# Kernel tuning notes

Hardware: AMD Instinct MI355X
Metric: run time of the kernel (lower is better)

Reference implementation:

```python
import jax, jax.numpy as jnp
import numpy as np
import math

EMBED_DIM = 1024
N1 = 8192
N2 = 8192

def setup_inputs() -> dict:
    key = jax.random.key(0)
    ks = jax.random.split(key, 16)
    D = EMBED_DIM
    s = 1.0 / math.sqrt(D)
    inp = {
        "input_tensor1": jax.random.normal(ks[0], (N1, D), jnp.float32),
        "input_tensor2": jax.random.normal(ks[1], (N2, D), jnp.float32),
    }
    names = ["q1", "k1", "v1", "q2", "k2", "v2"]
    for i, n in enumerate(names):
        inp[f"W{n}"] = jax.random.normal(ks[2 + 2 * i], (D, D), jnp.float32) * s
        inp[f"b{n}"] = jax.random.normal(ks[3 + 2 * i], (D,), jnp.float32) * 0.01
    return inp

def reference(input_tensor1, input_tensor2,
              Wq1, bq1, Wk1, bk1, Wv1, bv1,
              Wq2, bq2, Wk2, bk2, Wv2, bv2):
    D = Wq1.shape[0]
    scale = 1.0 / math.sqrt(D)
    # projections (torch Linear: x @ W^T + b; here W stored pre-transposed)
    q1 = input_tensor1 @ Wq1 + bq1   # [N1, D]
    k1 = input_tensor1 @ Wk1 + bk1   # [N1, D]
    v1 = input_tensor1 @ Wv1 + bv1   # [N1, D]
    q2 = input_tensor2 @ Wq2 + bq2   # [N2, D]
    k2 = input_tensor2 @ Wk2 + bk2   # [N2, D]
    v2 = input_tensor2 @ Wv2 + bv2   # [N2, D]
    # direction 1: tensor2 queries attend to tensor1 keys/values
    probs1 = jax.nn.sigmoid((q2 @ k1.T) * scale)   # [N2, N1]
    ctx1 = probs1 @ v1                              # [N2, D]
    # direction 2: tensor1 queries attend to tensor2 keys/values
    probs2 = jax.nn.sigmoid((q1 @ k2.T) * scale)   # [N1, N2]
    ctx2 = probs2 @ v2                              # [N1, D]
    return (ctx2, probs2, ctx1, probs1)
```

## Files before the change

### kernel.cpp

```cpp
#include <hip/hip_runtime.h>
#include <hip/hip_bf16.h>

#define DIM   1024
#define NTOK  8192

using bf16 = __hip_bfloat16;
typedef __attribute__((ext_vector_type(8))) short bf16x8;
typedef __attribute__((ext_vector_type(4))) float f32x4;

__device__ __forceinline__ unsigned short f2b(float x) {
  union { __hip_bfloat16 h; unsigned short u; } cv;
  cv.h = __float2bfloat16(x);
  return cv.u;
}

__global__ __launch_bounds__(256) void cast_f32_bf16(const float* __restrict__ in,
                                                     bf16* __restrict__ out, int n4) {
  int i = blockIdx.x * 256 + threadIdx.x;
  if (i < n4) {
    const float4 v = ((const float4*)in)[i];
    ushort4 p;
    p.x = f2b(v.x); p.y = f2b(v.y); p.z = f2b(v.z); p.w = f2b(v.w);
    ((ushort4*)out)[i] = p;
  }
}

__global__ __launch_bounds__(256) void transpose_cast32(const float* __restrict__ in,
                                                        bf16* __restrict__ out, int R, int C) {
  __shared__ float t[32][33];
  const int tilesC = C / 32;
  const int c0 = (blockIdx.x % tilesC) * 32;
  const int r0 = (blockIdx.x / tilesC) * 32;
  const int tx = threadIdx.x & 31, ty = threadIdx.x >> 5;
  #pragma unroll
  for (int i = 0; i < 4; ++i) {
    int r = ty + i * 8;
    t[r][tx] = in[(size_t)(r0 + r) * C + c0 + tx];
  }
  __syncthreads();
  #pragma unroll
  for (int i = 0; i < 4; ++i) {
    int cr = ty + i * 8;
    out[(size_t)(c0 + cr) * R + r0 + tx] = __float2bfloat16(t[tx][cr]);
  }
}

__global__ __launch_bounds__(256) void transpose_bf16(const short* __restrict__ in,
                                                      short* __restrict__ out,
                                                      const short* __restrict__ in2,
                                                      short* __restrict__ out2,
                                                      int R, int C) {
  __shared__ short t[64][72];
  const int tilesC = C >> 6;
  const int tilesPer = (R >> 6) * tilesC;
  int bid = blockIdx.x;
  const short* src = in; short* dst = out;
  if (bid >= tilesPer) { bid -= tilesPer; src = in2; dst = out2; }
  const int r0 = (bid / tilesC) << 6, c0 = (bid % tilesC) << 6;
  const int tr = threadIdx.x >> 3, tc8 = (threadIdx.x & 7) << 3;
  #pragma unroll
  for (int p = 0; p < 2; ++p) {
    int r = tr + p * 32;
    int sc = tc8 ^ (((r >> 3) & 7) << 3);
    *(bf16x8*)&t[r][sc] = *(const bf16x8*)&src[(size_t)(r0 + r) * C + c0 + tc8];
  }
  __syncthreads();
  #pragma unroll
  for (int p = 0; p < 2; ++p) {
    int oc = tr + p * 32;
    bf16x8 v;
    #pragma unroll
    for (int e = 0; e < 8; ++e) {
      int a = tc8 + e;
      v[e] = t[a][oc ^ (((a >> 3) & 7) << 3)];
    }
    *(bf16x8*)&dst[(size_t)(c0 + oc) * R + r0 + tc8] = v;
  }
}

__global__ __launch_bounds__(256) void pack_bias(const float* b0, const float* b1,
                                                 const float* b2, const float* b3,
                                                 const float* b4, const float* b5,
                                                 float* __restrict__ out) {
  int i = blockIdx.x * 256 + threadIdx.x;
  if (i < 6 * DIM) {
    int s = i >> 10, o = i & 1023;
    const float* p = (s == 0) ? b0 : (s == 1) ? b1 : (s == 2) ? b2 : (s == 3) ? b3 : (s == 4) ? b4 : b5;
    out[i] = p[o];
  }
}

template<int EPI, bool DUAL>
__global__ __launch_bounds__(256, 3) void gemm128(
    const bf16* __restrict__ A,  const bf16* __restrict__ Bt,
    const bf16* __restrict__ A2, const bf16* __restrict__ Bt2,
    int M, int N, int K, int TM, int perDir,
    const float* __restrict__ bias, const float* __restrict__ bias2, float scale,
    float* __restrict__ Cf, float* __restrict__ Cf2,
    bf16* __restrict__ Cb, bf16* __restrict__ Cb2,
    bf16* __restrict__ Cq, bf16* __restrict__ Ck, bf16* __restrict__ Cv,
    bf16* __restrict__ Cq2, bf16* __restrict__ Ck2, bf16* __restrict__ Cv2)
{
  __shared__ __align__(16) char smem[49152];
  bf16* sA = (bf16*)smem;
  bf16* sB = (bf16*)(smem + 24576);
  float* Lf = (float*)smem;

  const int t    = threadIdx.x;
  const int lane = t & 63, wid = t >> 6;
  const int wr = wid >> 1, wc = wid & 1;
  const int lr = lane & 15, kg = lane >> 4;

  const int nwg = gridDim.x;
  int bid = blockIdx.x;
  { const int q = nwg >> 3; bid = (bid & 7) * q + (bid >> 3); }

  const bf16* Au = A; const bf16* BtU = Bt;
  float* CfU = Cf; bf16* CbU = Cb;
  if (DUAL && bid >= perDir) { bid -= perDir; Au = A2; BtU = Bt2; CfU = Cf2; CbU = Cb2; }

  const int gw = TM << 3;
  const int s  = bid / gw, w = bid % gw;
  const int bm = (w >> 3) << 7;
  const int bn = ((s << 3) + (w & 7)) << 7;

  const float* biasU = bias;
  bf16 *CqU = Cq, *CkU = Ck, *CvU = Cv;
  int bmL = bm;
  if (EPI == 5 && bm >= (M >> 1)) {
    BtU = Bt2; biasU = bias2; CqU = Cq2; CkU = Ck2; CvU = Cv2; bmL = bm - (M >> 1);
  }

  const int srow = t >> 2;
  const int scol = ((t & 3) ^ ((t >> 3) & 3)) * 8;
  const size_t gA = (size_t)(bm + srow) * K + scol;
  const size_t gB = (size_t)(bn + srow) * K + scol;

#define STAGE(slot, isB, R0, tt_) \
  __builtin_amdgcn_global_load_lds( \
    (const __attribute__((address_space(1))) unsigned int*)(((isB) ? BtU + gB : Au + gA) + (size_t)(R0) * K + (size_t)(tt_) * 32), \
    (__attribute__((address_space(3))) unsigned int*)(((isB) ? sB : sA) + (slot) * 4096 + (R0) * 32 + t * 8), \
    16, 0, 0)

  const int swz  = (kg ^ ((lr >> 1) & 3)) * 8;
  const int aoff = (wr * 64 + lr) * 32 + swz;
  const int boff = (wc * 64 + lr) * 32 + swz;

  f32x4 acc[4][4] = {};
  const int NT = K >> 5;

  STAGE(0, 0, 0, 0); STAGE(0, 0, 64, 0); STAGE(0, 1, 0, 0); STAGE(0, 1, 64, 0);
  STAGE(1, 0, 0, 1); STAGE(1, 0, 64, 1); STAGE(1, 1, 0, 1); STAGE(1, 1, 64, 1);
  asm volatile("s_waitcnt vmcnt(4)" ::: "memory");
  __builtin_amdgcn_sched_barrier(0);
  __builtin_amdgcn_s_barrier();

  int cur = 0, stg = 2;
  for (int tt = 0; tt < NT; ++tt) {
    bf16x8 a[4], b[4];
    const bf16* pa = sA + cur * 4096 + aoff;
    const bf16* pb = sB + cur * 4096 + boff;
    #pragma unroll
    for (int i = 0; i < 4; ++i) a[i] = *(const bf16x8*)(pa + i * 512);
    #pragma unroll
    for (int i = 0; i < 4; ++i) b[i] = *(const bf16x8*)(pb + i * 512);
    if (tt + 2 < NT) {
      STAGE(stg, 0, 0, tt + 2); STAGE(stg, 0, 64, tt + 2);
      STAGE(stg, 1, 0, tt + 2); STAGE(stg, 1, 64, tt + 2);
    }
    __builtin_amdgcn_s_barrier();
    asm volatile("s_waitcnt lgkmcnt(0)" ::: "memory");
    __builtin_amdgcn_sched_barrier(0);
    __builtin_amdgcn_s_setprio(1);
    #pragma unroll
    for (int mi = 0; mi < 4; ++mi)
      #pragma unroll
      for (int n = 0; n < 4; ++n)
        acc[mi][n] = __builtin_amdgcn_mfma_f32_16x16x32_bf16(a[mi], b[n], acc[mi][n], 0, 0, 0);
    __builtin_amdgcn_s_setprio(0);
    if (tt + 2 < NT) { asm volatile("s_waitcnt vmcnt(4)" ::: "memory"); }
    else             { asm volatile("s_waitcnt vmcnt(0)" ::: "memory"); }
    __builtin_amdgcn_sched_barrier(0);
    __builtin_amdgcn_s_barrier();
    cur = (cur == 2) ? 0 : cur + 1;
    stg = (stg == 2) ? 0 : stg + 1;
  }
#undef STAGE

  float bv[4];
  if (EPI == 5) {
    #pragma unroll
    for (int n = 0; n < 4; ++n) bv[n] = biasU[bn + wc * 64 + n * 16 + lr];
  }

  #pragma unroll
  for (int h = 0; h < 2; ++h) {
    if (wr == h) {
      #pragma unroll
      for (int mi = 0; mi < 4; ++mi)
        #pragma unroll
        for (int n = 0; n < 4; ++n)
          #pragma unroll
          for (int e = 0; e < 4; ++e) {
            const int lrow = mi * 16 + kg * 4 + e;
            const int lcol = wc * 64 + n * 16 + lr;
            float v = acc[mi][n][e];
            if (EPI == 2 || EPI == 4) v = 1.0f / (1.0f + __expf(-v * scale));
            if (EPI == 5) v += bv[n];
            Lf[lrow * 128 + lcol] = v;
          }
    }
    __syncthreads();
    #pragma unroll
    for (int rr = 0; rr < 8; ++rr) {
      const int lrow = wid * 16 + rr * 2 + (lane >> 5);
      const int col  = (lane & 31) * 4;
      const f32x4 v = *(const f32x4*)&Lf[lrow * 128 + col];
      const int gr = bm + h * 64 + lrow;
      if (EPI == 2 || EPI == 4) {
        __builtin_nontemporal_store(v, (f32x4*)&CfU[(size_t)gr * N + bn + col]);
        if (EPI == 4) {
          ushort4 p; p.x = f2b(v[0]); p.y = f2b(v[1]); p.z = f2b(v[2]); p.w = f2b(v[3]);
          *(ushort4*)&CbU[(size_t)gr * N + bn + col] = p;
        }
      } else if (EPI == 3) {
        __builtin_nontemporal_store(v, (f32x4*)&CfU[(size_t)gr * N + bn + col]);
      } else if (EPI == 5) {
        const int seg = bn >> 10;
        const int cl  = (bn & 1023) + col;
        const int r   = bmL + h * 64 + lrow;
        bf16* sel = (seg == 0) ? CqU : (seg == 1) ? CkU : CvU;
        ushort4 p; p.x = f2b(v[0]); p.y = f2b(v[1]); p.z = f2b(v[2]); p.w = f2b(v[3]);
        *(ushort4*)&sel[(size_t)r * DIM + cl] = p;
      }
    }
    __syncthreads();
  }
}

template<int EPI, bool A_F32>
__global__ __launch_bounds__(256) void gemm_nt(
    const void* __restrict__ Ap, const bf16* __restrict__ Bt,
    int M, int N, int K,
    float scale, float* __restrict__ Cf)
{
  __shared__ bf16 As[128 * 32];
  __shared__ bf16 Bs[128 * 32];
  const int tid  = threadIdx.x;
  const int lane = tid & 63, wid = tid >> 6;
  const int wrr = wid >> 1, wcc = wid & 1;
  const int tilesN = N >> 7;
  const int nwg = gridDim.x;
  int bid = blockIdx.x;
  if ((nwg & 7) == 0) { const int q = nwg >> 3; bid = (bid & 7) * q + (bid >> 3); }
  const int bm = (bid / tilesN) * 128, bn = (bid % tilesN) * 128;
  f32x4 acc[4][4] = {};
  const bf16*  Ab16 = (const bf16*)Ap;
  const float* Af32 = (const float*)Ap;
  const int srow = tid >> 2, sc8 = (tid & 3) * 8;
  const int frow = tid >> 3, fc4 = (tid & 7) * 4;

  for (int k0 = 0; k0 < K; k0 += 32) {
    if (A_F32) {
      #pragma unroll
      for (int is = 0; is < 4; ++is) {
        int row = is * 32 + frow;
        const float4 v = *(const float4*)(Af32 + (size_t)(bm + row) * K + k0 + fc4);
        ushort4 p; p.x = f2b(v.x); p.y = f2b(v.y); p.z = f2b(v.z); p.w = f2b(v.w);
        *(ushort4*)(&As[row * 32 + fc4]) = p;
      }
    } else {
      #pragma unroll
      for (int is = 0; is < 2; ++is) {
        int row = is * 64 + srow;
        const bf16* g = Ab16 + (size_t)(bm + row) * K + k0 + sc8;
        __builtin_amdgcn_global_load_lds(
            (const __attribute__((address_space(1))) unsigned int*)g,
            (__attribute__((address_space(3))) unsigned int*)(&As[row * 32 + sc8]), 16, 0, 0);
      }
    }
    #pragma unroll
    for (int is = 0; is < 2; ++is) {
      int row = is * 64 + srow;
      const bf16* g = Bt + (size_t)(bn + row) * K + k0 + sc8;
      __builtin_amdgcn_global_load_lds(
          (const __attribute__((address_space(1))) unsigned int*)g,
          (__attribute__((address_space(3))) unsigned int*)(&Bs[row * 32 + sc8]), 16, 0, 0);
    }
    __syncthreads();
    const int lrr = lane & 15, kgg = lane >> 4;
    bf16x8 af[4], bfv[4];
    #pragma unroll
    for (int i = 0; i < 4; ++i)
      af[i] = *(const bf16x8*)(&As[(wrr * 64 + i * 16 + lrr) * 32 + kgg * 8]);
    #pragma unroll
    for (int j = 0; j < 4; ++j)
      bfv[j] = *(const bf16x8*)(&Bs[(wcc * 64 + j * 16 + lrr) * 32 + kgg * 8]);
    #pragma unroll
    for (int i = 0; i < 4; ++i)
      #pragma unroll
      for (int j = 0; j < 4; ++j)
        acc[i][j] = __builtin_amdgcn_mfma_f32_16x16x32_bf16(af[i], bfv[j], acc[i][j], 0, 0, 0);
    __syncthreads();
  }
  const int r0 = bm + wrr * 64 + (lane >> 4) * 4;
  const int c0 = bn + wcc * 64 + (lane & 15);
  if (EPI == 2) {
    #pragma unroll
    for (int i = 0; i < 4; ++i)
      #pragma unroll
      for (int j = 0; j < 4; ++j)
        #pragma unroll
        for (int e = 0; e < 4; ++e) {
          float pr = 1.0f / (1.0f + __expf(-acc[i][j][e] * scale));
          Cf[(size_t)(r0 + i * 16 + e) * N + c0 + j * 16] = pr;
        }
  } else {
    #pragma unroll
    for (int i = 0; i < 4; ++i)
      #pragma unroll
      for (int j = 0; j < 4; ++j)
        #pragma unroll
        for (int e = 0; e < 4; ++e)
          Cf[(size_t)(r0 + i * 16 + e) * N + c0 + j * 16] = acc[i][j][e];
  }
}

extern "C" void kernel_launch(void* const* d_in, const int* in_sizes, int n_in,
                              void* d_out, int out_size, void* d_ws, size_t ws_size,
                              hipStream_t stream) {
  const float* x1 = (const float*)d_in[0];
  const float* x2 = (const float*)d_in[1];
  const float* W[6] = { (const float*)d_in[2],  (const float*)d_in[4],  (const float*)d_in[6],
                        (const float*)d_in[8],  (const float*)d_in[10], (const float*)d_in[12] };
  const float* B[6] = { (const float*)d_in[3],  (const float*)d_in[5],  (const float*)d_in[7],
                        (const float*)d_in[9],  (const float*)d_in[11], (const float*)d_in[13] };

  const size_t MD = (size_t)NTOK * DIM;
  const size_t DD = (size_t)DIM * DIM;
  const size_t NN = (size_t)NTOK * NTOK;

  bf16* ws   = (bf16*)d_ws;
  bf16* x1b  = ws;
  bf16* x2b  = x1b + MD;
  bf16* wt1  = x2b + MD;
  bf16* wt2  = wt1 + 3 * DD;
  float* bstack = (float*)(wt2 + 3 * DD);
  bf16* q1   = wt2 + 3 * DD + 16384;
  bf16* k1   = q1 + MD;
  bf16* q2   = k1 + MD;
  bf16* k2   = q2 + MD;
  bf16* v1r  = k2 + MD;
  bf16* v2r  = v1r + MD;
  bf16* v1T  = v2r + MD;
  bf16* v2T  = v1T + MD;
  bf16* probsb = v2T + MD;

  const size_t topBytes = ((size_t)(10 * MD + 6 * DD + 16384) + 2 * NN) * 2;
  const bool top = (ws_size >= topBytes);

  float* out    = (float*)d_out;
  float* ctx2   = out;
  float* probs2 = ctx2 + MD;
  float* ctx1   = probs2 + NN;
  float* probs1 = ctx1 + MD;

  const float scale = 1.0f / 32.0f;

  {
    int n4 = (int)(MD / 4);
    int blks = (n4 + 255) / 256;
    cast_f32_bf16<<<blks, 256, 0, stream>>>(x1, x1b, n4);
    cast_f32_bf16<<<blks, 256, 0, stream>>>(x2, x2b, n4);
  }
  {
    int blks = (DIM / 32) * (DIM / 32);
    transpose_cast32<<<blks, 256, 0, stream>>>(W[0], wt1 + 0 * DD, DIM, DIM);
    transpose_cast32<<<blks, 256, 0, stream>>>(W[1], wt1 + 1 * DD, DIM, DIM);
    transpose_cast32<<<blks, 256, 0, stream>>>(W[2], wt1 + 2 * DD, DIM, DIM);
    transpose_cast32<<<blks, 256, 0, stream>>>(W[3], wt2 + 0 * DD, DIM, DIM);
    transpose_cast32<<<blks, 256, 0, stream>>>(W[4], wt2 + 1 * DD, DIM, DIM);
    transpose_cast32<<<blks, 256, 0, stream>>>(W[5], wt2 + 2 * DD, DIM, DIM);
  }
  pack_bias<<<24, 256, 0, stream>>>(B[0], B[1], B[2], B[3], B[4], B[5], bstack);

  gemm128<5, false><<<128 * 24, 256, 0, stream>>>(
      x1b, wt1, nullptr, wt2, 2 * NTOK, 3 * DIM, DIM, 128, 3072,
      bstack, bstack + 3 * DIM, 0.f,
      nullptr, nullptr, nullptr, nullptr,
      q1, k1, v1r, q2, k2, v2r);

  transpose_bf16<<<2 * (NTOK / 64) * (DIM / 64), 256, 0, stream>>>(
      (const short*)v1r, (short*)v1T, (const short*)v2r, (short*)v2T, NTOK, DIM);

  const int perQK = (NTOK / 128) * (NTOK / 128);
  const int perPV = (NTOK / 128) * (DIM / 128);

  if (top) {
    gemm128<4, true><<<2 * perQK, 256, 0, stream>>>(
        q1, k2, q2, k1, NTOK, NTOK, DIM, 64, perQK,
        nullptr, nullptr, scale,
        probs2, probs1, probsb, probsb + NN,
        nullptr, nullptr, nullptr, nullptr, nullptr, nullptr);
    gemm128<3, true><<<2 * perPV, 256, 0, stream>>>(
        probsb, v2T, probsb + NN, v1T, NTOK, DIM, NTOK, 64, perPV,
        nullptr, nullptr, 0.f,
        ctx2, ctx1, nullptr, nullptr,
        nullptr, nullptr, nullptr, nullptr, nullptr, nullptr);
  } else {
    gemm128<2, false><<<perQK, 256, 0, stream>>>(
        q1, k2, nullptr, nullptr, NTOK, NTOK, DIM, 64, perQK,
        nullptr, nullptr, scale,
        probs2, nullptr, nullptr, nullptr,
        nullptr, nullptr, nullptr, nullptr, nullptr, nullptr);
    gemm_nt<3, true><<<(NTOK / 128) * (DIM / 128), 256, 0, stream>>>(
        probs2, v2T, NTOK, DIM, NTOK, 0.f, ctx2);
    gemm128<2, false><<<perQK, 256, 0, stream>>>(
        q2, k1, nullptr, nullptr, NTOK, NTOK, DIM, 64, perQK,
        nullptr, nullptr, scale,
        probs1, nullptr, nullptr, nullptr,
        nullptr, nullptr, nullptr, nullptr, nullptr, nullptr);
    gemm_nt<3, true><<<(NTOK / 128) * (DIM / 128), 256, 0, stream>>>(
        probs1, v1T, NTOK, DIM, NTOK, 0.f, ctx1);
  }
}
```

Before: 879.7 us.

## Emit fp32 probabilities from PV GEMM's staged bf16 tiles instead of QK epilogue

The QK GEMM now stores only bf16 sigmoid probabilities. The PV GEMM converts its LDS-resident bf16 A tiles back to fp32 and streams them out as the fp32 probs output, with each column block writing a disjoint slice of K. This moves the large fp32 write out of the QK epilogue so it can overlap with PV MFMA work. In exchange, the fp32 probs are now bf16-rounded, and the extra stores inside the PV main loop may disturb its pipelining.

Measured after the change: 1.168 ms. 32.8% more time.

```diff
diff --git a/kernel.cpp b/kernel.cpp
--- a/kernel.cpp
+++ b/kernel.cpp
@@ -12,6 +12,10 @@
   union { __hip_bfloat16 h; unsigned short u; } cv;
   cv.h = __float2bfloat16(x);
   return cv.u;
+}
+__device__ __forceinline__ float b2f(short s) {
+  unsigned u = ((unsigned)(unsigned short)s) << 16;
+  float f; __builtin_memcpy(&f, &u, 4); return f;
 }
 
 __global__ __launch_bounds__(256) void cast_f32_bf16(const float* __restrict__ in,
@@ -98,6 +102,7 @@
     const float* __restrict__ bias, const float* __restrict__ bias2, float scale,
     float* __restrict__ Cf, float* __restrict__ Cf2,
     bf16* __restrict__ Cb, bf16* __restrict__ Cb2,
+    float* __restrict__ Pf, float* __restrict__ Pf2,
     bf16* __restrict__ Cq, bf16* __restrict__ Ck, bf16* __restrict__ Cv,
     bf16* __restrict__ Cq2, bf16* __restrict__ Ck2, bf16* __restrict__ Cv2)
 {
@@ -116,13 +121,14 @@
   { const int q = nwg >> 3; bid = (bid & 7) * q + (bid >> 3); }
 
   const bf16* Au = A; const bf16* BtU = Bt;
-  float* CfU = Cf; bf16* CbU = Cb;
-  if (DUAL && bid >= perDir) { bid -= perDir; Au = A2; BtU = Bt2; CfU = Cf2; CbU = Cb2; }
+  float* CfU = Cf; bf16* CbU = Cb; float* PfU = Pf;
+  if (DUAL && bid >= perDir) { bid -= perDir; Au = A2; BtU = Bt2; CfU = Cf2; CbU = Cb2; PfU = Pf2; }
 
   const int gw = TM << 3;
   const int s  = bid / gw, w = bid % gw;
   const int bm = (w >> 3) << 7;
   const int bn = ((s << 3) + (w & 7)) << 7;
+  const int nj = bn >> 7;
 
   const float* biasU = bias;
   bf16 *CqU = Cq, *CkU = Ck, *CvU = Cv;
@@ -178,6 +184,25 @@
       for (int n = 0; n < 4; ++n)
         acc[mi][n] = __builtin_amdgcn_mfma_f32_16x16x32_bf16(a[mi], b[n], acc[mi][n], 0, 0, 0);
     __builtin_amdgcn_s_setprio(0);
+
+    if (EPI == 3 && (tt >> 5) == nj) {
+      const int r  = t >> 1;
+      const int pc = (t & 1) * 2;
+      const int xr = (r >> 1) & 3;
+      const bf16* src = sA + cur * 4096 + r * 32 + pc * 8;
+      float* dst = PfU + (size_t)(bm + r) * NTOK + tt * 32;
+      #pragma unroll
+      for (int c = 0; c < 2; ++c) {
+        bf16x8 v = *(const bf16x8*)(src + c * 8);
+        const int lcol = ((pc + c) ^ xr) * 8;
+        f32x4 lo, hi;
+        #pragma unroll
+        for (int e = 0; e < 4; ++e) { lo[e] = b2f(v[e]); hi[e] = b2f(v[4 + e]); }
+        __builtin_nontemporal_store(lo, (f32x4*)&dst[lcol]);
+        __builtin_nontemporal_store(hi, (f32x4*)&dst[lcol + 4]);
+      }
+    }
+
     if (tt + 2 < NT) { asm volatile("s_waitcnt vmcnt(4)" ::: "memory"); }
     else             { asm volatile("s_waitcnt vmcnt(0)" ::: "memory"); }
     __builtin_amdgcn_sched_barrier(0);
@@ -217,12 +242,11 @@
       const int col  = (lane & 31) * 4;
       const f32x4 v = *(const f32x4*)&Lf[lrow * 128 + col];
       const int gr = bm + h * 64 + lrow;
-      if (EPI == 2 || EPI == 4) {
+      if (EPI == 2) {
         __builtin_nontemporal_store(v, (f32x4*)&CfU[(size_t)gr * N + bn + col]);
-        if (EPI == 4) {
-          ushort4 p; p.x = f2b(v[0]); p.y = f2b(v[1]); p.z = f2b(v[2]); p.w = f2b(v[3]);
-          *(ushort4*)&CbU[(size_t)gr * N + bn + col] = p;
-        }
+      } else if (EPI == 4) {
+        ushort4 p; p.x = f2b(v[0]); p.y = f2b(v[1]); p.z = f2b(v[2]); p.w = f2b(v[3]);
+        *(ushort4*)&CbU[(size_t)gr * N + bn + col] = p;
       } else if (EPI == 3) {
         __builtin_nontemporal_store(v, (f32x4*)&CfU[(size_t)gr * N + bn + col]);
       } else if (EPI == 5) {
@@ -387,7 +411,7 @@
   gemm128<5, false><<<128 * 24, 256, 0, stream>>>(
       x1b, wt1, nullptr, wt2, 2 * NTOK, 3 * DIM, DIM, 128, 3072,
       bstack, bstack + 3 * DIM, 0.f,
-      nullptr, nullptr, nullptr, nullptr,
+      nullptr, nullptr, nullptr, nullptr, nullptr, nullptr,
       q1, k1, v1r, q2, k2, v2r);
 
   transpose_bf16<<<2 * (NTOK / 64) * (DIM / 64), 256, 0, stream>>>(
@@ -400,25 +424,25 @@
     gemm128<4, true><<<2 * perQK, 256, 0, stream>>>(
         q1, k2, q2, k1, NTOK, NTOK, DIM, 64, perQK,
         nullptr, nullptr, scale,
-        probs2, probs1, probsb, probsb + NN,
+        nullptr, nullptr, probsb, probsb + NN, nullptr, nullptr,
         nullptr, nullptr, nullptr, nullptr, nullptr, nullptr);
     gemm128<3, true><<<2 * perPV, 256, 0, stream>>>(
         probsb, v2T, probsb + NN, v1T, NTOK, DIM, NTOK, 64, perPV,
         nullptr, nullptr, 0.f,
-        ctx2, ctx1, nullptr, nullptr,
+        ctx2, ctx1, nullptr, nullptr, probs2, probs1,
         nullptr, nullptr, nullptr, nullptr, nullptr, nullptr);
   } else {
     gemm128<2, false><<<perQK, 256, 0, stream>>>(
         q1, k2, nullptr, nullptr, NTOK, NTOK, DIM, 64, perQK,
         nullptr, nullptr, scale,
-        probs2, nullptr, nullptr, nullptr,
+        probs2, nullptr, nullptr, nullptr, nullptr, nullptr,
         nullptr, nullptr, nullptr, nullptr, nullptr, nullptr);
     gemm_nt<3, true><<<(NTOK / 128) * (DIM / 128), 256, 0, stream>>>(
         probs2, v2T, NTOK, DIM, NTOK, 0.f, ctx2);
     gemm128<2, false><<<perQK, 256, 0, stream>>>(
         q2, k1, nullptr, nullptr, NTOK, NTOK, DIM, 64, perQK,
         nullptr, nullptr, scale,
-        probs1, nullptr, nullptr, nullptr,
+        probs1, nullptr, nullptr, nullptr, nullptr, nullptr,
         nullptr, nullptr, nullptr, nullptr, nullptr, nullptr);
     gemm_nt<3, true><<<(NTOK / 128) * (DIM / 128), 256, 0, stream>>>(
         probs1, v1T, NTOK, DIM, NTOK, 0.f, ctx1);
```
